# Optimization experiments

Hardware: AMD Instinct MI355X
Metric: run time of the kernel (lower is better)

Reference implementation:

```python
import jax, jax.numpy as jnp
import numpy as np

N_EMBD = 1024
N_HEAD = 16
HEAD_DIM = N_EMBD // N_HEAD
WINDOW = 256


def setup_inputs() -> dict:
    key = jax.random.key(0)
    ks = jax.random.split(key, 9)
    B, T, C = 2, 2048, N_EMBD
    s = 1.0 / np.sqrt(C)
    inp = {
        'x': jax.random.normal(ks[0], (B, T, C), jnp.float32),
        'Wq': jax.random.normal(ks[1], (C, C), jnp.float32) * s,
        'bq': jnp.zeros((C,), jnp.float32),
        'Wk': jax.random.normal(ks[2], (C, C), jnp.float32) * s,
        'bk': jnp.zeros((C,), jnp.float32),
        'Wv': jax.random.normal(ks[3], (C, C), jnp.float32) * s,
        'bv': jnp.zeros((C,), jnp.float32),
        'Wo': jax.random.normal(ks[4], (C, C), jnp.float32) * s,
        'bo': jnp.zeros((C,), jnp.float32),
    }
    return inp


def reference(x, Wq, bq, Wk, bk, Wv, bv, Wo, bo):
    B, T, C = x.shape
    H, D = N_HEAD, HEAD_DIM
    # projections -> [B, H, T, D]
    q = (x @ Wq + bq).reshape(B, T, H, D).transpose(0, 2, 1, 3)
    k = (x @ Wk + bk).reshape(B, T, H, D).transpose(0, 2, 1, 3)
    v = (x @ Wv + bv).reshape(B, T, H, D).transpose(0, 2, 1, 3)
    # dense scores [B, H, T, T]
    scores = jnp.einsum('bhid,bhjd->bhij', q, k) / jnp.sqrt(jnp.float32(D))
    # sliding-window + causal mask: allow j <= i and i - j <= WINDOW
    i = jnp.arange(T)[:, None]
    j = jnp.arange(T)[None, :]
    mask = (j <= i) & (i - j <= WINDOW)  # [T, T]
    scores = jnp.where(mask[None, None], scores, -jnp.inf)
    probs = jax.nn.softmax(scores, axis=-1)
    out = jnp.einsum('bhij,bhjd->bhid', probs, v)  # [B,H,T,D]
    out = out.transpose(0, 2, 1, 3).reshape(B, T, C)
    return out @ Wo + bo
```

## Files before the change

kernel.cpp:

```cpp
#include <hip/hip_runtime.h>


typedef _Float16 f16;
typedef _Float16 half8 __attribute__((ext_vector_type(8)));
typedef _Float16 half4 __attribute__((ext_vector_type(4)));
typedef float    f32x4 __attribute__((ext_vector_type(4)));

#define MFMA16(a, b, c) __builtin_amdgcn_mfma_f32_16x16x32_f16((a), (b), (c), 0, 0, 0)

__device__ __forceinline__ void gload16(const void* g, void* l) {
  __builtin_amdgcn_global_load_lds(
      (const __attribute__((address_space(1))) void*)g,
      (__attribute__((address_space(3))) void*)l, 16, 0, 0);
}

#define BARX() do { asm volatile("" ::: "memory");  \
                    __builtin_amdgcn_s_barrier();   \
                    asm volatile("" ::: "memory"); } while (0)

__global__ __launch_bounds__(256) void prep_kernel(
    const float* __restrict__ x, f16* __restrict__ xb,
    const float* __restrict__ W0, const float* __restrict__ W1,
    const float* __restrict__ W2, const float* __restrict__ W3,
    f16* __restrict__ T0, f16* __restrict__ T1,
    f16* __restrict__ T2, f16* __restrict__ T3) {
  const int bid = blockIdx.x;
  if (bid < 2048) {
    const int idx = (bid * 256 + threadIdx.x) * 8;
    const float4 a = *(const float4*)(x + idx);
    const float4 b = *(const float4*)(x + idx + 4);
    half8 h;
    h[0] = (f16)a.x; h[1] = (f16)a.y; h[2] = (f16)a.z; h[3] = (f16)a.w;
    h[4] = (f16)b.x; h[5] = (f16)b.y; h[6] = (f16)b.z; h[7] = (f16)b.w;
    *(half8*)(xb + idx) = h;
    return;
  }
  __shared__ float tile[32][33];
  const int rem0 = bid - 2048;
  const int mat = rem0 >> 10;
  const int rem = rem0 & 1023;
  const int kt = (rem >> 5) * 32;
  const int nt = (rem & 31) * 32;
  const float* W = mat == 0 ? W0 : mat == 1 ? W1 : mat == 2 ? W2 : W3;
  f16* T = mat == 0 ? T0 : mat == 1 ? T1 : mat == 2 ? T2 : T3;
  const int tid = threadIdx.x;
  const int r = tid >> 3;
  const int c4 = (tid & 7) * 4;
  const float4 v = *(const float4*)(W + (size_t)(kt + r) * 1024 + nt + c4);
  tile[r][c4 + 0] = v.x; tile[r][c4 + 1] = v.y;
  tile[r][c4 + 2] = v.z; tile[r][c4 + 3] = v.w;
  __syncthreads();
  half4 o;
  #pragma unroll
  for (int e = 0; e < 4; e++) o[e] = (f16)tile[c4 + e][r];
  *(half4*)(T + (size_t)(nt + r) * 1024 + kt + c4) = o;
}

__global__ __launch_bounds__(512, 2) void gemm_qkv8_kernel(
    const f16* __restrict__ xb, const f16* __restrict__ wt,
    const float* __restrict__ bq, const float* __restrict__ bk,
    const float* __restrict__ bv,
    f16* __restrict__ qo, f16* __restrict__ ko, f16* __restrict__ vt) {
  __shared__ __align__(16) f16 sA[2][2][8192];
  __shared__ __align__(16) f16 sB[2][2][8192];

  const int tid = threadIdx.x;
  const int lane = tid & 63, wave = tid >> 6;
  const int wm = wave >> 2, wn = wave & 3;
  const int fr = lane & 15, fg = lane >> 4;
  const int sx = (fr & 7) << 4;

  const int wg = (blockIdx.x & 7) * 24 + (blockIdx.x >> 3);
  const int m0 = (wg & 15) * 256;
  const int n0 = (wg >> 4) * 256;

  const int row0 = tid >> 3;
  const int row1 = row0 + 64;
  const int cc = tid & 7;
  const size_t goff0 = (size_t)row0 * 1024 + (size_t)((cc ^ (row0 & 7)) * 8);
  const size_t goff1 = (size_t)row1 * 1024 + (size_t)((cc ^ (row1 & 7)) * 8);
  const int ldso0 = wave * 64 * 8;
  const int ldso1 = (512 + wave * 64) * 8;

  const f16* Abase = xb + (size_t)m0 * 1024;
  const f16* Bbase = wt + (size_t)n0 * 1024;

  auto stageA = [&](int par, int h, int t) {
    const f16* g = Abase + (size_t)h * 131072 + t * 64;
    f16* r = &sA[par][h][0];
    gload16(g + goff0, r + ldso0);
    gload16(g + goff1, r + ldso1);
  };
  auto stageB = [&](int par, int h, int t) {
    const f16* g = Bbase + (size_t)h * 131072 + t * 64;
    f16* r = &sB[par][h][0];
    gload16(g + goff0, r + ldso0);
    gload16(g + goff1, r + ldso1);
  };

  f32x4 acc[8][4];
  #pragma unroll
  for (int i = 0; i < 8; i++)
    #pragma unroll
    for (int j = 0; j < 4; j++) acc[i][j] = (f32x4){0.f, 0.f, 0.f, 0.f};

  half8 a[4][2], b0[2][2], b1[2][2];

  auto LDA = [&](int par, int qm) {
    const char* base = (const char*)&sA[par][qm][0];
    #pragma unroll
    for (int mf = 0; mf < 4; mf++)
      #pragma unroll
      for (int kk = 0; kk < 2; kk++)
        a[mf][kk] = *(const half8*)(
            base + ((((wm * 64 + mf * 16 + fr) * 128) + kk * 64 + fg * 16) ^ sx));
  };
  auto LDB = [&](int par, int qn, half8 (&b)[2][2]) {
    const char* base = (const char*)&sB[par][qn][0];
    #pragma unroll
    for (int nf = 0; nf < 2; nf++)
      #pragma unroll
      for (int kk = 0; kk < 2; kk++)
        b[nf][kk] = *(const half8*)(
            base + ((((wn * 32 + nf * 16 + fr) * 128) + kk * 64 + fg * 16) ^ sx));
  };
  auto MF = [&](int qm, int qn, half8 (&b)[2][2]) {
    __builtin_amdgcn_s_setprio(1);
    #pragma unroll
    for (int mf = 0; mf < 4; mf++)
      #pragma unroll
      for (int nf = 0; nf < 2; nf++)
        #pragma unroll
        for (int kk = 0; kk < 2; kk++)
          acc[qm * 4 + mf][qn * 2 + nf] =
              MFMA16(a[mf][kk], b[nf][kk], acc[qm * 4 + mf][qn * 2 + nf]);
    __builtin_amdgcn_s_setprio(0);
  };

  stageA(0, 0, 0); stageA(0, 1, 0); stageB(0, 0, 0); stageB(0, 1, 0);
  stageA(1, 0, 1); stageB(1, 0, 1);
  asm volatile("s_waitcnt vmcnt(4)" ::: "memory");
  BARX();

  for (int i = 0; i < 8; ++i) {
    const int t1 = 2 * i + 1;
    const bool more = (i < 7);
    LDA(0, 0); LDB(0, 0, b0);
    stageA(1, 1, t1);
    MF(0, 0, b0);
    BARX();
    LDB(0, 1, b1);
    stageB(1, 1, t1);
    MF(0, 1, b1);
    BARX();
    LDA(0, 1);
    if (more) stageA(0, 0, t1 + 1);
    MF(1, 0, b0);
    BARX();
    if (more) stageB(0, 0, t1 + 1);
    MF(1, 1, b1);
    if (more) { asm volatile("s_waitcnt vmcnt(4)" ::: "memory"); }
    else      { asm volatile("s_waitcnt vmcnt(0)" ::: "memory"); }
    BARX();
    LDA(1, 0); LDB(1, 0, b0);
    if (more) stageA(0, 1, t1 + 1);
    MF(0, 0, b0);
    BARX();
    LDB(1, 1, b1);
    if (more) stageB(0, 1, t1 + 1);
    MF(0, 1, b1);
    BARX();
    LDA(1, 1);
    if (more) stageA(1, 0, t1 + 2);
    MF(1, 0, b0);
    BARX();
    if (more) stageB(1, 0, t1 + 2);
    MF(1, 1, b1);
    if (more) { asm volatile("s_waitcnt vmcnt(4)" ::: "memory"); }
    else      { asm volatile("s_waitcnt vmcnt(0)" ::: "memory"); }
    BARX();
  }

  const int matid = n0 >> 10;
  const int nc0 = n0 & 1023;
  const float* bias = matid == 0 ? bq : matid == 1 ? bk : bv;
  if (matid < 2) {
    f16* out = matid == 0 ? qo : ko;
    #pragma unroll
    for (int qm = 0; qm < 2; qm++)
      #pragma unroll
      for (int mf = 0; mf < 4; mf++)
        #pragma unroll
        for (int qn = 0; qn < 2; qn++)
          #pragma unroll
          for (int nf = 0; nf < 2; nf++) {
            const int col = nc0 + qn * 128 + wn * 32 + nf * 16 + fr;
            const float bb = bias[col];
            #pragma unroll
            for (int r = 0; r < 4; r++) {
              const int row = m0 + qm * 128 + wm * 64 + mf * 16 + fg * 4 + r;
              out[(size_t)row * 1024 + col] =
                  (f16)(acc[qm * 4 + mf][qn * 2 + nf][r] + bb);
            }
          }
  } else {
    #pragma unroll
    for (int qm = 0; qm < 2; qm++)
      #pragma unroll
      for (int mf = 0; mf < 4; mf++)
        #pragma unroll
        for (int qn = 0; qn < 2; qn++)
          #pragma unroll
          for (int nf = 0; nf < 2; nf++) {
            const int row = m0 + qm * 128 + wm * 64 + mf * 16 + fg * 4;
            const int col = nc0 + qn * 128 + wn * 32 + nf * 16 + fr;
            const int b = row >> 11, t = row & 2047;
            const int h = col >> 6, d = col & 63;
            const float bb = bias[col];
            half4 vv;
            #pragma unroll
            for (int r = 0; r < 4; r++)
              vv[r] = (f16)(acc[qm * 4 + mf][qn * 2 + nf][r] + bb);
            *(half4*)(vt + (((size_t)(b * 16 + h)) * 64 + d) * 2048 + t) = vv;
          }
  }
}

__device__ __forceinline__ void gemm_tile(const f16* __restrict__ A,
                                          const f16* __restrict__ Bt,
                                          int m0, int n0,
                                          f16* As, f16* Bs,
                                          f32x4 acc[4][4]) {
  const int tid = threadIdx.x;
  const int lane = tid & 63;
  const int wave = tid >> 6;
  const int wm = (wave >> 1) * 64;
  const int wn = (wave & 1) * 64;
  const int r4 = lane >> 2;
  const int c8 = (lane & 3) * 8;
  const int fr = lane & 15;
  const int fg = lane >> 4;
  const int ch = wave * 2;

  const f16* a0 = A + (size_t)(m0 + ch * 16 + r4) * 1024 + c8;
  const f16* a1 = a0 + (size_t)16 * 1024;
  const f16* b0 = Bt + (size_t)(n0 + ch * 16 + r4) * 1024 + c8;
  const f16* b1 = b0 + (size_t)16 * 1024;

  #pragma unroll
  for (int mf = 0; mf < 4; mf++)
    #pragma unroll
    for (int nf = 0; nf < 4; nf++) acc[mf][nf] = (f32x4){0.f, 0.f, 0.f, 0.f};

  gload16(a0, As + ch * 512);
  gload16(a1, As + ch * 512 + 512);
  gload16(b0, Bs + ch * 512);
  gload16(b1, Bs + ch * 512 + 512);
  __syncthreads();

  for (int it = 0; it < 32; ++it) {
    const int cur = it & 1;
    if (it < 31) {
      const int kt = (it + 1) * 32;
      f16* An = As + (cur ^ 1) * 4096;
      f16* Bn = Bs + (cur ^ 1) * 4096;
      gload16(a0 + kt, An + ch * 512);
      gload16(a1 + kt, An + ch * 512 + 512);
      gload16(b0 + kt, Bn + ch * 512);
      gload16(b1 + kt, Bn + ch * 512 + 512);
    }
    const f16* Ac = As + cur * 4096;
    const f16* Bc = Bs + cur * 4096;
    half8 af[4], bf[4];
    #pragma unroll
    for (int mf = 0; mf < 4; mf++)
      af[mf] = *(const half8*)(Ac + (wm + mf * 16 + fr) * 32 + fg * 8);
    #pragma unroll
    for (int nf = 0; nf < 4; nf++)
      bf[nf] = *(const half8*)(Bc + (wn + nf * 16 + fr) * 32 + fg * 8);
    #pragma unroll
    for (int mf = 0; mf < 4; mf++)
      #pragma unroll
      for (int nf = 0; nf < 4; nf++)
        acc[mf][nf] = MFMA16(af[mf], bf[nf], acc[mf][nf]);
    __syncthreads();
  }
}

__global__ __launch_bounds__(256, 3) void gemm_o_kernel(
    const f16* __restrict__ ao, const f16* __restrict__ wot,
    const float* __restrict__ bo, float* __restrict__ out) {
  __shared__ __align__(16) f16 As[2 * 4096];
  __shared__ __align__(16) f16 Bs[2 * 4096];
  const int bid = blockIdx.x;
  const int m0 = (bid & 31) * 128;
  const int n0 = (bid >> 5) * 128;
  f32x4 acc[4][4];
  gemm_tile(ao, wot, m0, n0, As, Bs, acc);
  const int lane = threadIdx.x & 63;
  const int wave = threadIdx.x >> 6;
  const int wm = (wave >> 1) * 64, wn = (wave & 1) * 64;
  const int fr = lane & 15, fg = lane >> 4;
  #pragma unroll
  for (int mf = 0; mf < 4; mf++)
    #pragma unroll
    for (int nf = 0; nf < 4; nf++)
      #pragma unroll
      for (int r = 0; r < 4; r++) {
        const int row = m0 + wm + mf * 16 + fg * 4 + r;
        const int col = n0 + wn + nf * 16 + fr;
        out[(size_t)row * 1024 + col] = acc[mf][nf][r] + bo[col];
      }
}

__global__ __launch_bounds__(256, 3) void attn_kernel(
    const f16* __restrict__ Q, const f16* __restrict__ K,
    const f16* __restrict__ Vt, f16* __restrict__ Ao) {
  __shared__ __align__(16) f16 Ks[2][64 * 64];
  __shared__ __align__(16) f16 Vs[2][64 * 64];
  __shared__ __align__(16) f16 Ps[4][16][72];

  const int tid = threadIdx.x, lane = tid & 63, wave = tid >> 6;
  const int fr = lane & 15, g = lane >> 4;
  const int qt = blockIdx.x & 31, bh = blockIdx.x >> 5;
  const int b = bh >> 4, h = bh & 15;
  const int q0 = qt * 64;
  const int qr = q0 + wave * 16;

  const f16* Qb = Q + ((size_t)(b * 2048 + qr)) * 1024 + h * 64;
  const half8 q0f = *(const half8*)(Qb + (size_t)fr * 1024 + g * 8);
  const half8 q1f = *(const half8*)(Qb + (size_t)fr * 1024 + 32 + g * 8);

  const char* Kg = (const char*)(K + ((size_t)(b * 2048)) * 1024 + h * 64);
  const char* Vg = (const char*)(Vt + ((size_t)(b * 16 + h)) * 64 * 2048);

  const int sr0 = wave * 16 + (lane >> 3);
  const int sr1 = sr0 + 8;
  const int sc = lane & 7;
  const int sco0 = (sc ^ (sr0 & 7)) << 4;
  const int sco1 = (sc ^ (sr1 & 7)) << 4;

  auto stageKV = [&](int buf, int jt) {
    gload16(Kg + (size_t)(jt + sr0) * 2048 + sco0, (f16*)Ks[buf] + wave * 1024);
    gload16(Kg + (size_t)(jt + sr1) * 2048 + sco1,
            (f16*)Ks[buf] + wave * 1024 + 512);
    gload16(Vg + (size_t)sr0 * 4096 + (size_t)jt * 2 + sco0,
            (f16*)Vs[buf] + wave * 1024);
    gload16(Vg + (size_t)sr1 * 4096 + (size_t)jt * 2 + sco1,
            (f16*)Vs[buf] + wave * 1024 + 512);
  };

  const int t0 = qt >= 4 ? qt - 4 : 0;
  const int t1 = qt;

  f32x4 O[4];
  #pragma unroll
  for (int nt = 0; nt < 4; nt++) O[nt] = (f32x4){0.f, 0.f, 0.f, 0.f};
  float lsum[4] = {0.f, 0.f, 0.f, 0.f};

  stageKV(0, t0 * 64);
  __syncthreads();

  for (int tt = t0; tt <= t1; ++tt) {
    const int cur = (tt - t0) & 1;
    if (tt < t1) stageKV(cur ^ 1, (tt + 1) * 64);
    const int jt = tt * 64;
    const bool alive = (jt <= qr + 15) && (jt + 63 >= qr - 256);
    if (alive) {
      const char* Kb = (const char*)Ks[cur];
      const char* Vb = (const char*)Vs[cur];
      f32x4 s[4];
      #pragma unroll
      for (int jj = 0; jj < 4; ++jj) {
        const int kj = jj * 16 + fr;
        const char* krow = Kb + kj * 128;
        const int kswz = (kj & 7) << 4;
        const half8 kf0 = *(const half8*)(krow + ((g * 16) ^ kswz));
        const half8 kf1 = *(const half8*)(krow + ((64 + g * 16) ^ kswz));
        s[jj] = (f32x4){0.f, 0.f, 0.f, 0.f};
        s[jj] = MFMA16(q0f, kf0, s[jj]);
        s[jj] = MFMA16(q1f, kf1, s[jj]);
      }
      const int eb0 = qr + g * 4 - jt - fr;
      #pragma unroll
      for (int jj = 0; jj < 4; ++jj) {
        #pragma unroll
        for (int r = 0; r < 4; ++r) {
          const float a = __expf(s[jj][r] * 0.125f - 3.0f);
          const float p = ((unsigned)(eb0 + r - jj * 16) <= 256u) ? a : 0.f;
          lsum[r] += p;
          Ps[wave][g * 4 + r][jj * 16 + fr] = (f16)p;
        }
      }
      #pragma unroll
      for (int ks = 0; ks < 2; ++ks) {
        const half8 pa = *(const half8*)(&Ps[wave][fr][ks * 32 + g * 8]);
        #pragma unroll
        for (int nt = 0; nt < 4; ++nt) {
          const int vd = nt * 16 + fr;
          const half8 vf = *(const half8*)(
              Vb + vd * 128 + ((ks * 64 + g * 16) ^ ((vd & 7) << 4)));
          O[nt] = MFMA16(pa, vf, O[nt]);
        }
      }
    }
    __syncthreads();
  }

  float inv[4];
  #pragma unroll
  for (int r = 0; r < 4; ++r) {
    float s = lsum[r];
    s += __shfl_xor(s, 1);
    s += __shfl_xor(s, 2);
    s += __shfl_xor(s, 4);
    s += __shfl_xor(s, 8);
    inv[r] = 1.0f / s;
  }
  f16* Aout = Ao + ((size_t)(b * 2048 + qr)) * 1024 + h * 64;
  #pragma unroll
  for (int nt = 0; nt < 4; ++nt)
    #pragma unroll
    for (int r = 0; r < 4; ++r)
      Aout[(size_t)(g * 4 + r) * 1024 + nt * 16 + fr] =
          (f16)(O[nt][r] * inv[r]);
}

extern "C" void kernel_launch(void* const* d_in, const int* in_sizes, int n_in,
                              void* d_out, int out_size, void* d_ws,
                              size_t ws_size, hipStream_t stream) {
  const float* x  = (const float*)d_in[0];
  const float* Wq = (const float*)d_in[1];
  const float* bq = (const float*)d_in[2];
  const float* Wk = (const float*)d_in[3];
  const float* bk = (const float*)d_in[4];
  const float* Wv = (const float*)d_in[5];
  const float* bv = (const float*)d_in[6];
  const float* Wo = (const float*)d_in[7];
  const float* bo = (const float*)d_in[8];

  char* w = (char*)d_ws;
  f16* xb  = (f16*)(w);
  f16* wqt = (f16*)(w + ((size_t)8 << 20));
  f16* wkt = (f16*)(w + ((size_t)10 << 20));
  f16* wvt = (f16*)(w + ((size_t)12 << 20));
  f16* wot = (f16*)(w + ((size_t)14 << 20));
  f16* q   = (f16*)(w + ((size_t)16 << 20));
  f16* kk  = (f16*)(w + ((size_t)24 << 20));
  f16* vt  = (f16*)(w + ((size_t)32 << 20));
  f16* ao  = (f16*)(w + ((size_t)40 << 20));

  prep_kernel<<<6144, 256, 0, stream>>>(x, xb, Wq, Wk, Wv, Wo,
                                        wqt, wkt, wvt, wot);
  gemm_qkv8_kernel<<<192, 512, 0, stream>>>(xb, wqt, bq, bk, bv, q, kk, vt);
  attn_kernel<<<1024, 256, 0, stream>>>(q, kk, vt, ao);
  gemm_o_kernel<<<256, 256, 0, stream>>>(ao, wot, bo, (float*)d_out);
}
```

Measured before the change: 90.82 us.

## Replace pipelined 256x256 QKV GEMM with shared single-buffered 128x128 GEMM core

Drops the hand-pipelined 256x256-tile QKV GEMM, with its double-buffered LDS and interleaved barriers, in favour of a simple 128x128-tile, K=64-step GEMM core. The same core is reused for the output projection, which moves from 256 to 512 threads with swizzled LDS and XCD-aware block remapping. The QKV launch grows from 192 to 768 blocks for more occupancy and CU coverage. In exchange there is no load/compute overlap inside a block (a single buffer with a sync before and after each step) and less data reuse per tile.

```diff
diff --git a/kernel.cpp b/kernel.cpp
--- a/kernel.cpp
+++ b/kernel.cpp
@@ -13,10 +13,6 @@
       (const __attribute__((address_space(1))) void*)g,
       (__attribute__((address_space(3))) void*)l, 16, 0, 0);
 }
-
-#define BARX() do { asm volatile("" ::: "memory");  \
-                    __builtin_amdgcn_s_barrier();   \
-                    asm volatile("" ::: "memory"); } while (0)
 
 __global__ __launch_bounds__(256) void prep_kernel(
     const float* __restrict__ x, f16* __restrict__ xb,
@@ -56,261 +52,142 @@
   *(half4*)(T + (size_t)(nt + r) * 1024 + kt + c4) = o;
 }
 
-__global__ __launch_bounds__(512, 2) void gemm_qkv8_kernel(
+__device__ __forceinline__ void gemm_core(const f16* __restrict__ A,
+                                          const f16* __restrict__ Bt,
+                                          int m0, int n0,
+                                          f16* As, f16* Bs,
+                                          f32x4 acc[4][2]) {
+  const int tid = threadIdx.x;
+  const int lane = tid & 63, wave = tid >> 6;
+  const int wm = wave >> 2, wn = wave & 3;
+  const int fr = lane & 15, fg = lane >> 4;
+
+  const int srow = wave * 16 + (lane >> 3);
+  const int cc = lane & 7;
+  const size_t go = (size_t)srow * 1024 + (size_t)((cc ^ (srow & 7)) * 8);
+  const f16* ag = A + (size_t)m0 * 1024 + go;
+  const f16* bg = Bt + (size_t)n0 * 1024 + go;
+  f16* la = As + wave * 1024;
+  f16* lb = Bs + wave * 1024;
+
+  #pragma unroll
+  for (int i = 0; i < 4; i++)
+    #pragma unroll
+    for (int j = 0; j < 2; j++) acc[i][j] = (f32x4){0.f, 0.f, 0.f, 0.f};
+
+  for (int kt = 0; kt < 1024; kt += 64) {
+    gload16(ag + kt, la);
+    gload16(ag + kt + 8192, la + 512);
+    gload16(bg + kt, lb);
+    gload16(bg + kt + 8192, lb + 512);
+    __syncthreads();
+    const char* Ab = (const char*)As;
+    const char* Bb = (const char*)Bs;
+    half8 af[4][2], bf[2][2];
+    #pragma unroll
+    for (int mf = 0; mf < 4; mf++) {
+      const int row = wm * 64 + mf * 16 + fr;
+      const int sw = (row & 7) << 4;
+      #pragma unroll
+      for (int kk = 0; kk < 2; kk++)
+        af[mf][kk] = *(const half8*)(Ab + row * 128 + ((kk * 64 + fg * 16) ^ sw));
+    }
+    #pragma unroll
+    for (int nf = 0; nf < 2; nf++) {
+      const int row = wn * 32 + nf * 16 + fr;
+      const int sw = (row & 7) << 4;
+      #pragma unroll
+      for (int kk = 0; kk < 2; kk++)
+        bf[nf][kk] = *(const half8*)(Bb + row * 128 + ((kk * 64 + fg * 16) ^ sw));
+    }
+    #pragma unroll
+    for (int mf = 0; mf < 4; mf++)
+      #pragma unroll
+      for (int nf = 0; nf < 2; nf++)
+        #pragma unroll
+        for (int kk = 0; kk < 2; kk++)
+          acc[mf][nf] = MFMA16(af[mf][kk], bf[nf][kk], acc[mf][nf]);
+    __syncthreads();
+  }
+}
+
+__global__ __launch_bounds__(512, 4) void gemm_qkv_kernel(
     const f16* __restrict__ xb, const f16* __restrict__ wt,
     const float* __restrict__ bq, const float* __restrict__ bk,
     const float* __restrict__ bv,
     f16* __restrict__ qo, f16* __restrict__ ko, f16* __restrict__ vt) {
-  __shared__ __align__(16) f16 sA[2][2][8192];
-  __shared__ __align__(16) f16 sB[2][2][8192];
-
-  const int tid = threadIdx.x;
-  const int lane = tid & 63, wave = tid >> 6;
+  __shared__ __align__(16) f16 As[128 * 64];
+  __shared__ __align__(16) f16 Bs[128 * 64];
+  const int wg = (blockIdx.x & 7) * 96 + (blockIdx.x >> 3);
+  const int m0 = (wg & 31) * 128;
+  const int n0 = (wg >> 5) * 128;
+  f32x4 acc[4][2];
+  gemm_core(xb, wt, m0, n0, As, Bs, acc);
+
+  const int lane = threadIdx.x & 63, wave = threadIdx.x >> 6;
   const int wm = wave >> 2, wn = wave & 3;
   const int fr = lane & 15, fg = lane >> 4;
-  const int sx = (fr & 7) << 4;
-
-  const int wg = (blockIdx.x & 7) * 24 + (blockIdx.x >> 3);
-  const int m0 = (wg & 15) * 256;
-  const int n0 = (wg >> 4) * 256;
-
-  const int row0 = tid >> 3;
-  const int row1 = row0 + 64;
-  const int cc = tid & 7;
-  const size_t goff0 = (size_t)row0 * 1024 + (size_t)((cc ^ (row0 & 7)) * 8);
-  const size_t goff1 = (size_t)row1 * 1024 + (size_t)((cc ^ (row1 & 7)) * 8);
-  const int ldso0 = wave * 64 * 8;
-  const int ldso1 = (512 + wave * 64) * 8;
-
-  const f16* Abase = xb + (size_t)m0 * 1024;
-  const f16* Bbase = wt + (size_t)n0 * 1024;
-
-  auto stageA = [&](int par, int h, int t) {
-    const f16* g = Abase + (size_t)h * 131072 + t * 64;
-    f16* r = &sA[par][h][0];
-    gload16(g + goff0, r + ldso0);
-    gload16(g + goff1, r + ldso1);
-  };
-  auto stageB = [&](int par, int h, int t) {
-    const f16* g = Bbase + (size_t)h * 131072 + t * 64;
-    f16* r = &sB[par][h][0];
-    gload16(g + goff0, r + ldso0);
-    gload16(g + goff1, r + ldso1);
-  };
-
-  f32x4 acc[8][4];
-  #pragma unroll
-  for (int i = 0; i < 8; i++)
-    #pragma unroll
-    for (int j = 0; j < 4; j++) acc[i][j] = (f32x4){0.f, 0.f, 0.f, 0.f};
-
-  half8 a[4][2], b0[2][2], b1[2][2];
-
-  auto LDA = [&](int par, int qm) {
-    const char* base = (const char*)&sA[par][qm][0];
-    #pragma unroll
-    for (int mf = 0; mf < 4; mf++)
-      #pragma unroll
-      for (int kk = 0; kk < 2; kk++)
-        a[mf][kk] = *(const half8*)(
-            base + ((((wm * 64 + mf * 16 + fr) * 128) + kk * 64 + fg * 16) ^ sx));
-  };
-  auto LDB = [&](int par, int qn, half8 (&b)[2][2]) {
-    const char* base = (const char*)&sB[par][qn][0];
-    #pragma unroll
-    for (int nf = 0; nf < 2; nf++)
-      #pragma unroll
-      for (int kk = 0; kk < 2; kk++)
-        b[nf][kk] = *(const half8*)(
-            base + ((((wn * 32 + nf * 16 + fr) * 128) + kk * 64 + fg * 16) ^ sx));
-  };
-  auto MF = [&](int qm, int qn, half8 (&b)[2][2]) {
-    __builtin_amdgcn_s_setprio(1);
-    #pragma unroll
-    for (int mf = 0; mf < 4; mf++)
-      #pragma unroll
-      for (int nf = 0; nf < 2; nf++)
-        #pragma unroll
-        for (int kk = 0; kk < 2; kk++)
-          acc[qm * 4 + mf][qn * 2 + nf] =
-              MFMA16(a[mf][kk], b[nf][kk], acc[qm * 4 + mf][qn * 2 + nf]);
-    __builtin_amdgcn_s_setprio(0);
-  };
-
-  stageA(0, 0, 0); stageA(0, 1, 0); stageB(0, 0, 0); stageB(0, 1, 0);
-  stageA(1, 0, 1); stageB(1, 0, 1);
-  asm volatile("s_waitcnt vmcnt(4)" ::: "memory");
-  BARX();
-
-  for (int i = 0; i < 8; ++i) {
-    const int t1 = 2 * i + 1;
-    const bool more = (i < 7);
-    LDA(0, 0); LDB(0, 0, b0);
-    stageA(1, 1, t1);
-    MF(0, 0, b0);
-    BARX();
-    LDB(0, 1, b1);
-    stageB(1, 1, t1);
-    MF(0, 1, b1);
-    BARX();
-    LDA(0, 1);
-    if (more) stageA(0, 0, t1 + 1);
-    MF(1, 0, b0);
-    BARX();
-    if (more) stageB(0, 0, t1 + 1);
-    MF(1, 1, b1);
-    if (more) { asm volatile("s_waitcnt vmcnt(4)" ::: "memory"); }
-    else      { asm volatile("s_waitcnt vmcnt(0)" ::: "memory"); }
-    BARX();
-    LDA(1, 0); LDB(1, 0, b0);
-    if (more) stageA(0, 1, t1 + 1);
-    MF(0, 0, b0);
-    BARX();
-    LDB(1, 1, b1);
-    if (more) stageB(0, 1, t1 + 1);
-    MF(0, 1, b1);
-    BARX();
-    LDA(1, 1);
-    if (more) stageA(1, 0, t1 + 2);
-    MF(1, 0, b0);
-    BARX();
-    if (more) stageB(1, 0, t1 + 2);
-    MF(1, 1, b1);
-    if (more) { asm volatile("s_waitcnt vmcnt(4)" ::: "memory"); }
-    else      { asm volatile("s_waitcnt vmcnt(0)" ::: "memory"); }
-    BARX();
-  }
-
   const int matid = n0 >> 10;
   const int nc0 = n0 & 1023;
   const float* bias = matid == 0 ? bq : matid == 1 ? bk : bv;
   if (matid < 2) {
     f16* out = matid == 0 ? qo : ko;
     #pragma unroll
-    for (int qm = 0; qm < 2; qm++)
-      #pragma unroll
-      for (int mf = 0; mf < 4; mf++)
-        #pragma unroll
-        for (int qn = 0; qn < 2; qn++)
-          #pragma unroll
-          for (int nf = 0; nf < 2; nf++) {
-            const int col = nc0 + qn * 128 + wn * 32 + nf * 16 + fr;
-            const float bb = bias[col];
-            #pragma unroll
-            for (int r = 0; r < 4; r++) {
-              const int row = m0 + qm * 128 + wm * 64 + mf * 16 + fg * 4 + r;
-              out[(size_t)row * 1024 + col] =
-                  (f16)(acc[qm * 4 + mf][qn * 2 + nf][r] + bb);
-            }
-          }
+    for (int mf = 0; mf < 4; mf++)
+      #pragma unroll
+      for (int nf = 0; nf < 2; nf++) {
+        const int col = nc0 + wn * 32 + nf * 16 + fr;
+        const float bb = bias[col];
+        #pragma unroll
+        for (int r = 0; r < 4; r++) {
+          const int row = m0 + wm * 64 + mf * 16 + fg * 4 + r;
+          out[(size_t)row * 1024 + col] = (f16)(acc[mf][nf][r] + bb);
+        }
+      }
   } else {
     #pragma unroll
-    for (int qm = 0; qm < 2; qm++)
-      #pragma unroll
-      for (int mf = 0; mf < 4; mf++)
-        #pragma unroll
-        for (int qn = 0; qn < 2; qn++)
-          #pragma unroll
-          for (int nf = 0; nf < 2; nf++) {
-            const int row = m0 + qm * 128 + wm * 64 + mf * 16 + fg * 4;
-            const int col = nc0 + qn * 128 + wn * 32 + nf * 16 + fr;
-            const int b = row >> 11, t = row & 2047;
-            const int h = col >> 6, d = col & 63;
-            const float bb = bias[col];
-            half4 vv;
-            #pragma unroll
-            for (int r = 0; r < 4; r++)
-              vv[r] = (f16)(acc[qm * 4 + mf][qn * 2 + nf][r] + bb);
-            *(half4*)(vt + (((size_t)(b * 16 + h)) * 64 + d) * 2048 + t) = vv;
-          }
-  }
-}
-
-__device__ __forceinline__ void gemm_tile(const f16* __restrict__ A,
-                                          const f16* __restrict__ Bt,
-                                          int m0, int n0,
-                                          f16* As, f16* Bs,
-                                          f32x4 acc[4][4]) {
-  const int tid = threadIdx.x;
-  const int lane = tid & 63;
-  const int wave = tid >> 6;
-  const int wm = (wave >> 1) * 64;
-  const int wn = (wave & 1) * 64;
-  const int r4 = lane >> 2;
-  const int c8 = (lane & 3) * 8;
-  const int fr = lane & 15;
-  const int fg = lane >> 4;
-  const int ch = wave * 2;
-
-  const f16* a0 = A + (size_t)(m0 + ch * 16 + r4) * 1024 + c8;
-  const f16* a1 = a0 + (size_t)16 * 1024;
-  const f16* b0 = Bt + (size_t)(n0 + ch * 16 + r4) * 1024 + c8;
-  const f16* b1 = b0 + (size_t)16 * 1024;
-
-  #pragma unroll
-  for (int mf = 0; mf < 4; mf++)
-    #pragma unroll
-    for (int nf = 0; nf < 4; nf++) acc[mf][nf] = (f32x4){0.f, 0.f, 0.f, 0.f};
-
-  gload16(a0, As + ch * 512);
-  gload16(a1, As + ch * 512 + 512);
-  gload16(b0, Bs + ch * 512);
-  gload16(b1, Bs + ch * 512 + 512);
-  __syncthreads();
-
-  for (int it = 0; it < 32; ++it) {
-    const int cur = it & 1;
-    if (it < 31) {
-      const int kt = (it + 1) * 32;
-      f16* An = As + (cur ^ 1) * 4096;
-      f16* Bn = Bs + (cur ^ 1) * 4096;
-      gload16(a0 + kt, An + ch * 512);
-      gload16(a1 + kt, An + ch * 512 + 512);
-      gload16(b0 + kt, Bn + ch * 512);
-      gload16(b1 + kt, Bn + ch * 512 + 512);
-    }
-    const f16* Ac = As + cur * 4096;
-    const f16* Bc = Bs + cur * 4096;
-    half8 af[4], bf[4];
-    #pragma unroll
     for (int mf = 0; mf < 4; mf++)
-      af[mf] = *(const half8*)(Ac + (wm + mf * 16 + fr) * 32 + fg * 8);
-    #pragma unroll
-    for (int nf = 0; nf < 4; nf++)
-      bf[nf] = *(const half8*)(Bc + (wn + nf * 16 + fr) * 32 + fg * 8);
-    #pragma unroll
-    for (int mf = 0; mf < 4; mf++)
-      #pragma unroll
-      for (int nf = 0; nf < 4; nf++)
-        acc[mf][nf] = MFMA16(af[mf], bf[nf], acc[mf][nf]);
-    __syncthreads();
-  }
-}
-
-__global__ __launch_bounds__(256, 3) void gemm_o_kernel(
+      #pragma unroll
+      for (int nf = 0; nf < 2; nf++) {
+        const int row = m0 + wm * 64 + mf * 16 + fg * 4;
+        const int col = nc0 + wn * 32 + nf * 16 + fr;
+        const int b = row >> 11, t = row & 2047;
+        const int h = col >> 6, d = col & 63;
+        const float bb = bias[col];
+        half4 vv;
+        #pragma unroll
+        for (int r = 0; r < 4; r++) vv[r] = (f16)(acc[mf][nf][r] + bb);
+        *(half4*)(vt + (((size_t)(b * 16 + h)) * 64 + d) * 2048 + t) = vv;
+      }
+  }
+}
+
+__global__ __launch_bounds__(512, 4) void gemm_o_kernel(
     const f16* __restrict__ ao, const f16* __restrict__ wot,
     const float* __restrict__ bo, float* __restrict__ out) {
-  __shared__ __align__(16) f16 As[2 * 4096];
-  __shared__ __align__(16) f16 Bs[2 * 4096];
-  const int bid = blockIdx.x;
-  const int m0 = (bid & 31) * 128;
-  const int n0 = (bid >> 5) * 128;
-  f32x4 acc[4][4];
-  gemm_tile(ao, wot, m0, n0, As, Bs, acc);
-  const int lane = threadIdx.x & 63;
-  const int wave = threadIdx.x >> 6;
-  const int wm = (wave >> 1) * 64, wn = (wave & 1) * 64;
+  __shared__ __align__(16) f16 As[128 * 64];
+  __shared__ __align__(16) f16 Bs[128 * 64];
+  const int wg = (blockIdx.x & 7) * 32 + (blockIdx.x >> 3);
+  const int m0 = (wg & 31) * 128;
+  const int n0 = (wg >> 5) * 128;
+  f32x4 acc[4][2];
+  gemm_core(ao, wot, m0, n0, As, Bs, acc);
+
+  const int lane = threadIdx.x & 63, wave = threadIdx.x >> 6;
+  const int wm = wave >> 2, wn = wave & 3;
   const int fr = lane & 15, fg = lane >> 4;
   #pragma unroll
   for (int mf = 0; mf < 4; mf++)
     #pragma unroll
-    for (int nf = 0; nf < 4; nf++)
+    for (int nf = 0; nf < 2; nf++) {
+      const int col = n0 + wn * 32 + nf * 16 + fr;
+      const float bb = bo[col];
       #pragma unroll
       for (int r = 0; r < 4; r++) {
-        const int row = m0 + wm + mf * 16 + fg * 4 + r;
-        const int col = n0 + wn + nf * 16 + fr;
-        out[(size_t)row * 1024 + col] = acc[mf][nf][r] + bo[col];
-      }
+        const int row = m0 + wm * 64 + mf * 16 + fg * 4 + r;
+        out[(size_t)row * 1024 + col] = acc[mf][nf][r] + bb;
+      }
+    }
 }
 
 __global__ __launch_bounds__(256, 3) void attn_kernel(
@@ -452,7 +329,7 @@
 
   prep_kernel<<<6144, 256, 0, stream>>>(x, xb, Wq, Wk, Wv, Wo,
                                         wqt, wkt, wvt, wot);
-  gemm_qkv8_kernel<<<192, 512, 0, stream>>>(xb, wqt, bq, bk, bv, q, kk, vt);
+  gemm_qkv_kernel<<<768, 512, 0, stream>>>(xb, wqt, bq, bk, bv, q, kk, vt);
   attn_kernel<<<1024, 256, 0, stream>>>(q, kk, vt, ao);
-  gemm_o_kernel<<<256, 256, 0, stream>>>(ao, wot, bo, (float*)d_out);
-}
+  gemm_o_kernel<<<256, 512, 0, stream>>>(ao, wot, bo, (float*)d_out);
+}
```

Result: faster. 84.65 us (-6.8%).
